# Performance work log

Measured on AMD Instinct MI355X. Metric: run time of the kernel, lower is better.

The kernel has to match this reference:

```python
import jax, jax.numpy as jnp
import numpy as np

V, E, H = 32000, 512, 1024
B, TS, TP = 32, 50, 32


def build_sparse_u_input(slot_np):
    # faithful jnp version of get_sparse_selective_input (vocab.decode EOS check skipped)
    ts, b = slot_np.shape
    res = jnp.full((ts, b, V + ts), 1e-10, dtype=jnp.float32)
    copy_mask = (slot_np == 2) | (slot_np >= V)
    add_mask = (slot_np != 0) & (~copy_mask)
    ti = jnp.arange(ts)[:, None]
    bi = jnp.arange(b)[None, :]
    res = res.at[ti, bi, slot_np].add(add_mask.astype(jnp.float32))
    res = res.at[ti, bi, V + ti].add((5.0 - 1e-10) * copy_mask.astype(jnp.float32))
    return jnp.transpose(res, (1, 0, 2))  # [B, Ts, V+Ts]


def setup_inputs() -> dict:
    key = jax.random.key(0)
    ks = jax.random.split(key, 20)
    s = lambda d: 1.0 / np.sqrt(d)
    slot_np = jax.random.randint(ks[0], (TS, B), 0, V)
    inp = {
        'slot_enc_out': jax.random.normal(ks[1], (TS, B, H), jnp.float32),
        'personality_enc_out': jax.random.normal(ks[2], (TP, B, H), jnp.float32),
        'last_hidden': jax.random.normal(ks[3], (1, B, H), jnp.float32),
        'm_t_input': jax.random.randint(ks[4], (1, B), 0, V),
        'slot_np': slot_np,
        'sparse_u_input': build_sparse_u_input(slot_np),
        'emb': jax.random.normal(ks[5], (V, E), jnp.float32),
        'W_attn_a': jax.random.normal(ks[6], (H, 2 * H), jnp.float32) * s(2 * H),
        'b_attn_a': jnp.zeros((H,), jnp.float32),
        'v_a': jax.random.normal(ks[7], (H,), jnp.float32) * s(H),
        'W_attn_p': jax.random.normal(ks[8], (H, 2 * H), jnp.float32) * s(2 * H),
        'b_attn_p': jnp.zeros((H,), jnp.float32),
        'v_p': jax.random.normal(ks[9], (H,), jnp.float32) * s(H),
        'W_ih': jax.random.normal(ks[10], (3 * H, E + 2 * H), jnp.float32) * s(E + 2 * H),
        'W_hh': jax.random.normal(ks[11], (3 * H, H), jnp.float32) * s(H),
        'b_ih': jnp.zeros((3 * H,), jnp.float32),
        'b_hh': jnp.zeros((3 * H,), jnp.float32),
        'W_proj': jax.random.normal(ks[12], (V, 3 * H), jnp.float32) * s(3 * H),
        'b_proj': jnp.zeros((V,), jnp.float32),
        'W_c2': jax.random.normal(ks[13], (H, H), jnp.float32) * s(H),
        'b_c2': jnp.zeros((H,), jnp.float32),
    }
    return inp


def _attn(hidden, enc, W, b, v):
    # hidden: [1,B,H], enc: [T,B,H] -> context [B,H]
    enc_b = jnp.swapaxes(enc, 0, 1)                       # [B,T,H]
    Hh = jnp.broadcast_to(hidden[0][:, None, :], enc_b.shape)
    e = jnp.tanh(jnp.concatenate([Hh, enc_b], -1) @ W.T + b)  # [B,T,H]
    a = jax.nn.softmax(jnp.einsum('bth,h->bt', e, v), axis=-1)
    return jnp.einsum('bt,bth->bh', a, enc_b)


def _gru_cell(x, h, W_ih, W_hh, b_ih, b_hh):
    gi = x @ W_ih.T + b_ih
    gh = h @ W_hh.T + b_hh
    ir, iz, inn = jnp.split(gi, 3, axis=-1)
    hr, hz, hn = jnp.split(gh, 3, axis=-1)
    r = jax.nn.sigmoid(ir + hr)
    z = jax.nn.sigmoid(iz + hz)
    n = jnp.tanh(inn + r * hn)
    return (1.0 - z) * n + z * h


def reference(slot_enc_out, personality_enc_out, last_hidden, m_t_input, slot_np,
              sparse_u_input, emb, W_attn_a, b_attn_a, v_a, W_attn_p, b_attn_p, v_p,
              W_ih, W_hh, b_ih, b_hh, W_proj, b_proj, W_c2, b_c2):
    m_embed = emb[m_t_input[0]]                                    # [B,E]
    a_ctx = _attn(last_hidden, slot_enc_out, W_attn_a, b_attn_a, v_a)
    p_ctx = _attn(last_hidden, personality_enc_out, W_attn_p, b_attn_p, v_p)
    gru_in = jnp.concatenate([m_embed, a_ctx, p_ctx], axis=-1)     # [B,E+2H]
    h_new = _gru_cell(gru_in, last_hidden[0], W_ih, W_hh, b_ih, b_hh)  # [B,H]
    gen_score = jnp.concatenate([a_ctx, p_ctx, h_new], -1) @ W_proj.T + b_proj  # [B,V]
    # copy score
    uc = jnp.tanh(jnp.swapaxes(slot_enc_out, 0, 1) @ W_c2.T + b_c2)  # [B,Ts,H]
    u = jnp.einsum('bth,bh->bt', uc, h_new)                          # [B,Ts]
    m = jnp.max(u, axis=1, keepdims=True)
    u = jnp.exp(u - m)
    u = jnp.log(jnp.einsum('bt,btv->bv', u, sparse_u_input)) + m     # [B,V+Ts]
    scores = jax.nn.softmax(jnp.concatenate([gen_score, u], axis=1), axis=1)
    gen, cp = scores[:, :V], scores[:, V:]
    proba = jnp.concatenate([gen + cp[:, :V], cp[:, V:]], axis=1)    # [B,V+Ts]
    return proba, h_new[None], h_new[None]
```

## Files before the change

### kernel.cpp

```cpp
#include <hip/hip_runtime.h>
#include <math.h>

static constexpr int V_   = 32000;
static constexpr int E_   = 512;
static constexpr int H_   = 1024;
static constexpr int B_   = 32;
static constexpr int TS_  = 50;
static constexpr int TP_  = 32;
static constexpr int VTS  = V_ + TS_;
static constexpr int H3   = 3 * H_;
static constexpr int GIN_ = E_ + 2 * H_;
static constexpr int NS   = 8;
static constexpr int SLE  = (VTS + NS - 1) / NS;
static constexpr int GSL  = V_ / NS;
static constexpr int PSK  = 12;

__global__ void zero_gather(float* __restrict__ extra,
                            const float* __restrict__ emb,
                            const int* __restrict__ mt,
                            float* __restrict__ gx)
{
    const int i = blockIdx.x * 256 + threadIdx.x;
    if (i < B_ * VTS) extra[i] = 0.f;
    if (i < B_ * E_) gx[i] = emb[(size_t)mt[i >> 9] * E_ + (i & 511)];
}

__device__ __forceinline__ void m32v2_tile(
    const float* __restrict__ A, int lda,
    const float* __restrict__ W, int ldw, int wko,
    int klen, int n0, float* __restrict__ po, int N)
{
    __shared__ float As[32][36];
    __shared__ float Ws[32][257];

    const int tid  = threadIdx.x;
    const int lane = tid & 63;
    const int wv   = tid >> 6;
    const int wq   = lane & 7;
    const int wg   = lane >> 3;
    const int am   = tid >> 3;
    const int aq   = tid & 7;

    float acc[8][4];
#pragma unroll
    for (int i = 0; i < 8; ++i)
#pragma unroll
        for (int j = 0; j < 4; ++j) acc[i][j] = 0.f;

    float4 a4 = *reinterpret_cast<const float4*>(A + (size_t)am * lda + 4 * aq);
    float4 w4[8];
#pragma unroll
    for (int i = 0; i < 8; ++i)
        w4[i] = *reinterpret_cast<const float4*>(
            W + (size_t)(n0 + wv * 64 + i * 8 + wg) * ldw + wko + 4 * wq);

    for (int kb = 0; kb < klen; kb += 32) {
        __syncthreads();
        As[4 * aq + 0][am] = a4.x; As[4 * aq + 1][am] = a4.y;
        As[4 * aq + 2][am] = a4.z; As[4 * aq + 3][am] = a4.w;
#pragma unroll
        for (int i = 0; i < 8; ++i) {
            const int col = wv * 64 + i * 8 + wg;
            Ws[4 * wq + 0][col] = w4[i].x; Ws[4 * wq + 1][col] = w4[i].y;
            Ws[4 * wq + 2][col] = w4[i].z; Ws[4 * wq + 3][col] = w4[i].w;
        }
        __syncthreads();
        if (kb + 32 < klen) {
            a4 = *reinterpret_cast<const float4*>(A + (size_t)am * lda + kb + 32 + 4 * aq);
#pragma unroll
            for (int i = 0; i < 8; ++i)
                w4[i] = *reinterpret_cast<const float4*>(
                    W + (size_t)(n0 + wv * 64 + i * 8 + wg) * ldw + wko + kb + 32 + 4 * wq);
        }
#pragma unroll 8
        for (int k = 0; k < 32; ++k) {
            const float4 a0 = *reinterpret_cast<const float4*>(&As[k][wv * 8]);
            const float4 a1 = *reinterpret_cast<const float4*>(&As[k][wv * 8 + 4]);
            const float av[8] = {a0.x, a0.y, a0.z, a0.w, a1.x, a1.y, a1.z, a1.w};
            const float w0 = Ws[k][lane];
            const float w1 = Ws[k][lane + 64];
            const float w2 = Ws[k][lane + 128];
            const float w3 = Ws[k][lane + 192];
#pragma unroll
            for (int i = 0; i < 8; ++i) {
                acc[i][0] = fmaf(av[i], w0, acc[i][0]);
                acc[i][1] = fmaf(av[i], w1, acc[i][1]);
                acc[i][2] = fmaf(av[i], w2, acc[i][2]);
                acc[i][3] = fmaf(av[i], w3, acc[i][3]);
            }
        }
    }
#pragma unroll
    for (int i = 0; i < 8; ++i) {
        float* op = po + (size_t)(wv * 8 + i) * N + n0;
#pragma unroll
        for (int j = 0; j < 4; ++j)
            op[lane + 64 * j] = acc[i][j];
    }
}

__global__ __launch_bounds__(256)
void gemm_hid(const float* __restrict__ hid,
              const float* __restrict__ Wa, const float* __restrict__ Wp,
              float* __restrict__ parts)
{
    const int z = blockIdx.z, y = blockIdx.y, n0 = blockIdx.x * 256;
    const float* W = z ? Wp : Wa;
    m32v2_tile(hid + y * 256, H_, W, 2 * H_, y * 256, 256, n0,
               parts + (size_t)(z * 4 + y) * B_ * H_, H_);
}

__global__ __launch_bounds__(256)
void gemm_pcg(const float* __restrict__ ctxa, const float* __restrict__ ctxp,
              const float* __restrict__ hid, const float* __restrict__ gx,
              const float* __restrict__ W_proj,
              const float* __restrict__ W_ih, const float* __restrict__ W_hh,
              float* __restrict__ partsP, float* __restrict__ partsG)
{
    const int bid = blockIdx.x;
    if (bid < 1000) {
        const int y = bid / 125, n0 = (bid % 125) * 256;
        const int slice = y >> 2, kq = y & 3;
        const float* A = slice ? ctxp : ctxa;
        m32v2_tile(A + kq * 256, H_, W_proj, H3, slice * 1024 + kq * 256,
                   256, n0, partsP + (size_t)y * B_ * V_, V_);
    } else {
        const int idx = bid - 1000;
        const int y = idx / 12, n0 = (idx % 12) * 256;
        const float* A; int lda; const float* W; int ldw; int wko; int klo;
        if (y < 2)       { klo = y * 256;        A = gx;   lda = E_; W = W_ih; ldw = GIN_; wko = klo; }
        else if (y < 6)  { klo = (y - 2) * 256;  A = ctxa; lda = H_; W = W_ih; ldw = GIN_; wko = 512 + klo; }
        else if (y < 10) { klo = (y - 6) * 256;  A = ctxp; lda = H_; W = W_ih; ldw = GIN_; wko = 1536 + klo; }
        else             { klo = (y - 10) * 256; A = hid;  lda = H_; W = W_hh; ldw = H_;   wko = klo; }
        m32v2_tile(A + klo, lda, W, ldw, wko, 256, n0,
                   partsG + (size_t)y * B_ * H3, H3);
    }
}

__global__ __launch_bounds__(256)
void gemm_projh(const float* __restrict__ hnew, const float* __restrict__ W_proj,
                float* __restrict__ partsP)
{
    const int y = blockIdx.y, n0 = blockIdx.x * 256;
    m32v2_tile(hnew + y * 256, H_, W_proj, H3, 2048 + y * 256,
               256, n0, partsP + (size_t)(8 + y) * B_ * V_, V_);
}

__global__ void reduce_gru(const float* __restrict__ parts,
                           const float* __restrict__ b_ih, const float* __restrict__ b_hh,
                           const float* __restrict__ hid,
                           float* __restrict__ hnew,
                           float* __restrict__ o2, float* __restrict__ o3)
{
    const int i = blockIdx.x * 256 + threadIdx.x;
    if (i >= B_ * H_) return;
    const int b = i >> 10, j = i & 1023;
    float gi[3], gh[3];
#pragma unroll
    for (int c = 0; c < 3; ++c) {
        float s = b_ih[c * H_ + j];
        for (int y = 0; y < 10; ++y)
            s += parts[((size_t)y * B_ + b) * H3 + c * H_ + j];
        gi[c] = s;
        float t = b_hh[c * H_ + j];
        for (int y = 10; y < 14; ++y)
            t += parts[((size_t)y * B_ + b) * H3 + c * H_ + j];
        gh[c] = t;
    }
    const float r = 1.f / (1.f + expf(-(gi[0] + gh[0])));
    const float z = 1.f / (1.f + expf(-(gi[1] + gh[1])));
    const float n = tanhf(gi[2] + r * gh[2]);
    const float o = (1.f - z) * n + z * hid[i];
    hnew[i] = o; o2[i] = o; o3[i] = o;
}

__global__ __launch_bounds__(256)
void gemm_tall84(const float* __restrict__ slot_enc, const float* __restrict__ pers_enc,
                 const float* __restrict__ W_attn_a, const float* __restrict__ W_attn_p,
                 const float* __restrict__ W_c2,
                 const float* __restrict__ b_attn_a, const float* __restrict__ b_attn_p,
                 const float* __restrict__ b_c2,
                 const float* __restrict__ v_a, const float* __restrict__ v_p,
                 const float* __restrict__ parts,
                 float* __restrict__ SA, float* __restrict__ SP, float* __restrict__ UCt)
{
    __shared__ float As[32][68];
    __shared__ float Ws[32][132];
    const int z = blockIdx.z;
    const float* A; const float* W; float* C; int M, ldw;
    if (z == 0)      { A = slot_enc; W = W_attn_a + H_; C = SA;  M = TS_ * B_; ldw = 2 * H_; }
    else if (z == 1) { A = pers_enc; W = W_attn_p + H_; C = SP;  M = TP_ * B_; ldw = 2 * H_; }
    else             { A = slot_enc; W = W_c2;          C = UCt; M = TS_ * B_; ldw = H_; }
    const int m0 = blockIdx.x * 64;
    if (m0 >= M) return;
    const int n0 = blockIdx.y * 128;
    const int tid = threadIdx.x;
    const int tym = tid >> 5;
    const int txn = tid & 31;
    const int sr = tid & 63, sh = tid >> 6;
    const int wr = tid & 127, wh = tid >> 7;

    float acc[8][4];
#pragma unroll
    for (int i = 0; i < 8; ++i)
#pragma unroll
        for (int j = 0; j < 4; ++j) acc[i][j] = 0.f;

    float4 a4[2], w4[4];
#pragma unroll
    for (int q = 0; q < 2; ++q)
        a4[q] = *reinterpret_cast<const float4*>(A + (size_t)(m0 + sr) * H_ + 8 * sh + 4 * q);
#pragma unroll
    for (int q = 0; q < 4; ++q)
        w4[q] = *reinterpret_cast<const float4*>(W + (size_t)(n0 + wr) * ldw + 16 * wh + 4 * q);

    for (int kb = 0; kb < H_; kb += 32) {
        __syncthreads();
#pragma unroll
        for (int q = 0; q < 2; ++q) {
            As[8 * sh + 4 * q + 0][sr] = a4[q].x; As[8 * sh + 4 * q + 1][sr] = a4[q].y;
            As[8 * sh + 4 * q + 2][sr] = a4[q].z; As[8 * sh + 4 * q + 3][sr] = a4[q].w;
        }
#pragma unroll
        for (int q = 0; q < 4; ++q) {
            Ws[16 * wh + 4 * q + 0][wr] = w4[q].x; Ws[16 * wh + 4 * q + 1][wr] = w4[q].y;
            Ws[16 * wh + 4 * q + 2][wr] = w4[q].z; Ws[16 * wh + 4 * q + 3][wr] = w4[q].w;
        }
        __syncthreads();
        if (kb + 32 < H_) {
#pragma unroll
            for (int q = 0; q < 2; ++q)
                a4[q] = *reinterpret_cast<const float4*>(A + (size_t)(m0 + sr) * H_ + kb + 32 + 8 * sh + 4 * q);
#pragma unroll
            for (int q = 0; q < 4; ++q)
                w4[q] = *reinterpret_cast<const float4*>(W + (size_t)(n0 + wr) * ldw + kb + 32 + 16 * wh + 4 * q);
        }
#pragma unroll 8
        for (int k = 0; k < 32; ++k) {
            const float4 a0 = *reinterpret_cast<const float4*>(&As[k][8 * tym]);
            const float4 a1 = *reinterpret_cast<const float4*>(&As[k][8 * tym + 4]);
            const float av[8] = {a0.x, a0.y, a0.z, a0.w, a1.x, a1.y, a1.z, a1.w};
            const float w0 = Ws[k][txn];
            const float w1 = Ws[k][txn + 32];
            const float w2 = Ws[k][txn + 64];
            const float w3 = Ws[k][txn + 96];
#pragma unroll
            for (int i = 0; i < 8; ++i) {
                acc[i][0] = fmaf(av[i], w0, acc[i][0]);
                acc[i][1] = fmaf(av[i], w1, acc[i][1]);
                acc[i][2] = fmaf(av[i], w2, acc[i][2]);
                acc[i][3] = fmaf(av[i], w3, acc[i][3]);
            }
        }
    }

    if (z < 2) {
        const float* bvec = z ? b_attn_p : b_attn_a;
        const float* vvec = z ? v_p : v_a;
        const float* pp = parts + (size_t)(z * 4) * B_ * H_;
#pragma unroll
        for (int i = 0; i < 8; ++i) {
            const int row = m0 + 8 * tym + i;
            const int b = row & 31;
#pragma unroll
            for (int j = 0; j < 4; ++j) {
                const int col = n0 + txn + 32 * j;
                float ha = bvec[col];
#pragma unroll
                for (int ss = 0; ss < 4; ++ss)
                    ha += pp[((size_t)ss * B_ + b) * H_ + col];
                C[(size_t)row * H_ + col] = tanhf(acc[i][j] + ha) * vvec[col];
            }
        }
    } else {
#pragma unroll
        for (int i = 0; i < 8; ++i) {
            const int row = m0 + 8 * tym + i;
#pragma unroll
            for (int j = 0; j < 4; ++j) {
                const int col = n0 + txn + 32 * j;
                C[(size_t)row * H_ + col] = tanhf(acc[i][j] + b_c2[col]);
            }
        }
    }
}

template <int T>
__device__ __forceinline__ void attn_body(const float* __restrict__ S,
                                          const float* __restrict__ enc,
                                          float* __restrict__ ctx, int b)
{
    const int tid  = threadIdx.x;
    const int wave = tid >> 6;
    const int lane = tid & 63;
    __shared__ float sc[64];
    __shared__ float aw[64];

    for (int t = wave; t < T; t += 8) {
        const float* e = S + ((size_t)t * B_ + b) * H_;
        float p = 0.f;
#pragma unroll
        for (int j = 0; j < H_ / 64; ++j) p += e[lane + 64 * j];
#pragma unroll
        for (int off = 32; off > 0; off >>= 1) p += __shfl_down(p, off);
        if (lane == 0) sc[t] = p;
    }
    __syncthreads();
    if (tid < 64) {
        const float x = (tid < T) ? sc[tid] : -3.4e38f;
        float mx = x;
#pragma unroll
        for (int off = 32; off > 0; off >>= 1) mx = fmaxf(mx, __shfl_xor(mx, off));
        const float ex = (tid < T) ? expf(x - mx) : 0.f;
        float sm = ex;
#pragma unroll
        for (int off = 32; off > 0; off >>= 1) sm += __shfl_xor(sm, off);
        aw[tid] = ex / sm;
    }
    __syncthreads();
    for (int k = tid; k < H_; k += 512) {
        float c = 0.f;
#pragma unroll 10
        for (int t = 0; t < T; ++t)
            c += aw[t] * enc[((size_t)t * B_ + b) * H_ + k];
        ctx[(size_t)b * H_ + k] = c;
    }
}

__global__ __launch_bounds__(512)
void attn_fused3(const float* __restrict__ SA, const float* __restrict__ SP,
                 const float* __restrict__ slot_enc, const float* __restrict__ pers_enc,
                 float* __restrict__ ctxa, float* __restrict__ ctxp)
{
    const int b = blockIdx.x;
    if (blockIdx.y == 0) attn_body<TS_>(SA, slot_enc, ctxa, b);
    else                 attn_body<TP_>(SP, pers_enc, ctxp, b);
}

__global__ __launch_bounds__(512)
void u_prep_scatter2(const float* __restrict__ UCt, const float* __restrict__ hn,
                     const int* __restrict__ slot_np,
                     float* __restrict__ mS, float* __restrict__ extra)
{
    const int b    = blockIdx.x;
    const int tid  = threadIdx.x;
    const int wave = tid >> 6;
    const int lane = tid & 63;
    __shared__ float su[64];
    __shared__ float eu_s[64];

    const float* h = hn + (size_t)b * H_;
    for (int t = wave; t < TS_; t += 8) {
        const float* r = UCt + ((size_t)t * B_ + b) * H_;
        float p = 0.f;
#pragma unroll
        for (int j = 0; j < H_ / 64; ++j)
            p += r[lane + 64 * j] * h[lane + 64 * j];
#pragma unroll
        for (int off = 32; off > 0; off >>= 1) p += __shfl_down(p, off);
        if (lane == 0) su[t] = p;
    }
    __syncthreads();
    if (tid < 64) {
        const float x = (tid < TS_) ? su[tid] : -3.4e38f;
        float mx = x;
#pragma unroll
        for (int off = 32; off > 0; off >>= 1) mx = fmaxf(mx, __shfl_xor(mx, off));
        const float ex = (tid < TS_) ? expf(x - mx) : 0.f;
        float sm = ex;
#pragma unroll
        for (int off = 32; off > 0; off >>= 1) sm += __shfl_xor(sm, off);
        eu_s[tid] = ex;
        if (tid == 0) { mS[b * 2] = mx; mS[b * 2 + 1] = sm; }
    }
    __syncthreads();
    if (tid < TS_) {
        const int sv = slot_np[tid * B_ + b];
        const float e = eu_s[tid];
        const bool copy = (sv == 2) || (sv >= V_);
        const bool add  = (sv != 0) && !copy;
        if (add)  atomicAdd(&extra[(size_t)b * VTS + sv], e);
        if (copy) atomicAdd(&extra[(size_t)b * VTS + V_ + tid], 5.0f * e);
    }
}

__device__ __forceinline__ float blk_reduce(float v, float* red, int tid, bool ismax)
{
    red[tid] = v; __syncthreads();
    for (int s = 128; s > 0; s >>= 1) {
        if (tid < s) red[tid] = ismax ? fmaxf(red[tid], red[tid + s]) : (red[tid] + red[tid + s]);
        __syncthreads();
    }
    const float r = red[0]; __syncthreads();
    return r;
}

__global__ __launch_bounds__(256)
void ph_max2g(const float* __restrict__ parts, const float* __restrict__ b_proj,
              const float* __restrict__ extra,
              float* __restrict__ gen,
              float* __restrict__ pgm, float* __restrict__ pzs,
              float* __restrict__ pem, float* __restrict__ pes)
{
    const int b = blockIdx.x, s = blockIdx.y, tid = threadIdx.x;
    __shared__ float red[256];
    const int g0 = s * GSL;

    float gv[16];
    float gm = -3.4e38f;
#pragma unroll
    for (int u = 0; u < 16; ++u) {
        const int loc = tid + 256 * u;
        float val = -3.4e38f;
        if (loc < GSL) {
            const int idx = g0 + loc;
            float ssum = 0.f;
#pragma unroll
            for (int ss = 0; ss < PSK; ++ss)
                ssum += parts[((size_t)ss * B_ + b) * V_ + idx];
            val = ssum + b_proj[idx];
            gen[(size_t)b * V_ + idx] = val;
            gm = fmaxf(gm, val);
        }
        gv[u] = val;
    }
    gm = blk_reduce(gm, red, tid, true);
    float zs = 0.f;
#pragma unroll
    for (int u = 0; u < 16; ++u)
        zs += expf(gv[u] - gm);
    zs = blk_reduce(zs, red, tid, false);

    const float* ex = extra + (size_t)b * VTS;
    const int e0 = s * SLE;
    const int e1 = (e0 + SLE < VTS) ? e0 + SLE : VTS;
    float em = 0.f, es = 0.f;
    for (int i = e0 + tid; i < e1; i += 256) { const float v = ex[i]; em = fmaxf(em, v); es += v; }
    em = blk_reduce(em, red, tid, true);
    es = blk_reduce(es, red, tid, false);
    if (tid == 0) {
        pgm[b * NS + s] = gm; pzs[b * NS + s] = zs;
        pem[b * NS + s] = em; pes[b * NS + s] = es;
    }
}

__global__ __launch_bounds__(256)
void ph_write2(const float* __restrict__ gen, const float* __restrict__ extra,
               const float* __restrict__ pgm, const float* __restrict__ pzs,
               const float* __restrict__ pem, const float* __restrict__ pes,
               const float* __restrict__ mS, float* __restrict__ proba)
{
    const int b = blockIdx.x, s = blockIdx.y, tid = threadIdx.x;
    const float mb   = mS[b * 2];
    const float Sb   = mS[b * 2 + 1];
    const float base = 1e-10f * Sb;

    float gm = -3.4e38f, em = 0.f;
#pragma unroll
    for (int k = 0; k < NS; ++k) {
        gm = fmaxf(gm, pgm[b * NS + k]);
        em = fmaxf(em, pem[b * NS + k]);
    }
    const float M = fmaxf(gm, mb + logf(base + em));
    float s1 = 0.f, s2 = 0.f;
#pragma unroll
    for (int k = 0; k < NS; ++k) {
        s1 += pzs[b * NS + k] * expf(pgm[b * NS + k] - M);
        s2 += pes[b * NS + k];
    }
    const float cs  = expf(mb - M);
    const float inv = 1.f / (s1 + cs * (base * VTS + s2));

    const float* g  = gen + (size_t)b * V_;
    const float* ex = extra + (size_t)b * VTS;
    float* o = proba + (size_t)b * VTS;
    const int e0 = s * SLE;
    const int e1 = (e0 + SLE < VTS) ? e0 + SLE : VTS;
    for (int i = e0 + tid; i < e1; i += 256) {
        const float cp = cs * (base + ex[i]) * inv;
        o[i] = (i < V_) ? (expf(g[i] - M) * inv + cp) : cp;
    }
}

extern "C" void kernel_launch(void* const* d_in, const int* in_sizes, int n_in,
                              void* d_out, int out_size, void* d_ws, size_t ws_size,
                              hipStream_t stream)
{
    const float* slot_enc = (const float*)d_in[0];
    const float* pers_enc = (const float*)d_in[1];
    const float* hid      = (const float*)d_in[2];
    const int*   mt       = (const int*)d_in[3];
    const int*   slot_np  = (const int*)d_in[4];
    const float* emb      = (const float*)d_in[6];
    const float* W_attn_a = (const float*)d_in[7];
    const float* b_attn_a = (const float*)d_in[8];
    const float* v_a      = (const float*)d_in[9];
    const float* W_attn_p = (const float*)d_in[10];
    const float* b_attn_p = (const float*)d_in[11];
    const float* v_p      = (const float*)d_in[12];
    const float* W_ih     = (const float*)d_in[13];
    const float* W_hh     = (const float*)d_in[14];
    const float* b_ih     = (const float*)d_in[15];
    const float* b_hh     = (const float*)d_in[16];
    const float* W_proj   = (const float*)d_in[17];
    const float* b_proj   = (const float*)d_in[18];
    const float* W_c2     = (const float*)d_in[19];
    const float* b_c2     = (const float*)d_in[20];
    float* out = (float*)d_out;

    float* w = (float*)d_ws;
    size_t off = 0;
    auto alloc = [&](size_t n) { float* p = w + off; off += n; return p; };
    float* SA    = alloc((size_t)TS_ * B_ * H_);
    float* SP    = alloc((size_t)TP_ * B_ * H_);
    float* UCt   = alloc((size_t)TS_ * B_ * H_);
    float* ctxa  = alloc((size_t)B_ * H_);
    float* ctxp  = alloc((size_t)B_ * H_);
    float* gx    = alloc((size_t)B_ * E_);
    float* hnew  = alloc((size_t)B_ * H_);
    float* gen   = alloc((size_t)B_ * V_);
    float* mS    = alloc((size_t)2 * B_);
    float* extra = alloc((size_t)B_ * VTS);
    float* pgm   = alloc((size_t)B_ * NS);
    float* pzs   = alloc((size_t)B_ * NS);
    float* pem   = alloc((size_t)B_ * NS);
    float* pes   = alloc((size_t)B_ * NS);
    float* partsP = alloc((size_t)PSK * B_ * V_);
    float* partsG = alloc((size_t)14 * B_ * H3);
    float* partsH = partsG;
    float* partsHd = alloc((size_t)8 * B_ * H_);

    const int o2 = B_ * VTS;
    const int o3 = o2 + B_ * H_;
    (void)partsH;

    zero_gather<<<(B_ * VTS + 255) / 256, 256, 0, stream>>>(extra, emb, mt, gx);

    gemm_hid<<<dim3(4, 4, 2), 256, 0, stream>>>(hid, W_attn_a, W_attn_p, partsHd);

    gemm_tall84<<<dim3(25, 8, 3), 256, 0, stream>>>(
        slot_enc, pers_enc, W_attn_a, W_attn_p, W_c2,
        b_attn_a, b_attn_p, b_c2, v_a, v_p, partsHd, SA, SP, UCt);

    attn_fused3<<<dim3(B_, 2), 512, 0, stream>>>(SA, SP, slot_enc, pers_enc, ctxa, ctxp);

    gemm_pcg<<<1168, 256, 0, stream>>>(ctxa, ctxp, hid, gx, W_proj, W_ih, W_hh, partsP, partsG);

    reduce_gru<<<(B_ * H_ + 255) / 256, 256, 0, stream>>>(partsG, b_ih, b_hh, hid, hnew, out + o2, out + o3);

    gemm_projh<<<dim3(125, 4), 256, 0, stream>>>(hnew, W_proj, partsP);

    u_prep_scatter2<<<B_, 512, 0, stream>>>(UCt, hnew, slot_np, mS, extra);

    ph_max2g<<<dim3(B_, NS), 256, 0, stream>>>(partsP, b_proj, extra, gen, pgm, pzs, pem, pes);
    ph_write2<<<dim3(B_, NS), 256, 0, stream>>>(gen, extra, pgm, pzs, pem, pes, mS, out);
}
```

Before: 403.7 us.

## Fuse small kernels and vectorize GEMM tile shared-memory reads and stores

```diff
diff --git a/kernel.cpp b/kernel.cpp
--- a/kernel.cpp
+++ b/kernel.cpp
@@ -14,16 +14,7 @@
 static constexpr int SLE  = (VTS + NS - 1) / NS;
 static constexpr int GSL  = V_ / NS;
 static constexpr int PSK  = 12;
-
-__global__ void zero_gather(float* __restrict__ extra,
-                            const float* __restrict__ emb,
-                            const int* __restrict__ mt,
-                            float* __restrict__ gx)
-{
-    const int i = blockIdx.x * 256 + threadIdx.x;
-    if (i < B_ * VTS) extra[i] = 0.f;
-    if (i < B_ * E_) gx[i] = emb[(size_t)mt[i >> 9] * E_ + (i & 511)];
-}
+static constexpr int NZB  = (B_ * VTS + 255) / 256;
 
 __device__ __forceinline__ void m32v2_tile(
     const float* __restrict__ A, int lda,
@@ -31,7 +22,7 @@
     int klen, int n0, float* __restrict__ po, int N)
 {
     __shared__ float As[32][36];
-    __shared__ float Ws[32][257];
+    __shared__ float Ws[32][256];
 
     const int tid  = threadIdx.x;
     const int lane = tid & 63;
@@ -77,37 +68,40 @@
             const float4 a0 = *reinterpret_cast<const float4*>(&As[k][wv * 8]);
             const float4 a1 = *reinterpret_cast<const float4*>(&As[k][wv * 8 + 4]);
             const float av[8] = {a0.x, a0.y, a0.z, a0.w, a1.x, a1.y, a1.z, a1.w};
-            const float w0 = Ws[k][lane];
-            const float w1 = Ws[k][lane + 64];
-            const float w2 = Ws[k][lane + 128];
-            const float w3 = Ws[k][lane + 192];
-#pragma unroll
-            for (int i = 0; i < 8; ++i) {
-                acc[i][0] = fmaf(av[i], w0, acc[i][0]);
-                acc[i][1] = fmaf(av[i], w1, acc[i][1]);
-                acc[i][2] = fmaf(av[i], w2, acc[i][2]);
-                acc[i][3] = fmaf(av[i], w3, acc[i][3]);
-            }
+            const float4 wf = *reinterpret_cast<const float4*>(&Ws[k][4 * lane]);
+            const float wvv[4] = {wf.x, wf.y, wf.z, wf.w};
+#pragma unroll
+            for (int i = 0; i < 8; ++i)
+#pragma unroll
+                for (int j = 0; j < 4; ++j)
+                    acc[i][j] = fmaf(av[i], wvv[j], acc[i][j]);
         }
     }
 #pragma unroll
     for (int i = 0; i < 8; ++i) {
-        float* op = po + (size_t)(wv * 8 + i) * N + n0;
-#pragma unroll
-        for (int j = 0; j < 4; ++j)
-            op[lane + 64 * j] = acc[i][j];
+        float4 o; o.x = acc[i][0]; o.y = acc[i][1]; o.z = acc[i][2]; o.w = acc[i][3];
+        *reinterpret_cast<float4*>(po + (size_t)(wv * 8 + i) * N + n0 + 4 * lane) = o;
     }
 }
 
 __global__ __launch_bounds__(256)
-void gemm_hid(const float* __restrict__ hid,
-              const float* __restrict__ Wa, const float* __restrict__ Wp,
-              float* __restrict__ parts)
-{
-    const int z = blockIdx.z, y = blockIdx.y, n0 = blockIdx.x * 256;
-    const float* W = z ? Wp : Wa;
-    m32v2_tile(hid + y * 256, H_, W, 2 * H_, y * 256, 256, n0,
-               parts + (size_t)(z * 4 + y) * B_ * H_, H_);
+void zg_hid(float* __restrict__ extra, const float* __restrict__ emb,
+            const int* __restrict__ mt, float* __restrict__ gx,
+            const float* __restrict__ hid,
+            const float* __restrict__ Wa, const float* __restrict__ Wp,
+            float* __restrict__ partsHd)
+{
+    const int bid = blockIdx.x;
+    if (bid < NZB) {
+        const int i = bid * 256 + threadIdx.x;
+        if (i < B_ * VTS) extra[i] = 0.f;
+        if (i < B_ * E_) gx[i] = emb[(size_t)mt[i >> 9] * E_ + (i & 511)];
+        return;
+    }
+    const int idx = bid - NZB;
+    const int z = idx >> 4, y = (idx >> 2) & 3, bx = idx & 3;
+    m32v2_tile(hid + y * 256, H_, z ? Wp : Wa, 2 * H_, y * 256, 256, bx * 256,
+               partsHd + (size_t)(z * 4 + y) * B_ * H_, H_);
 }
 
 __global__ __launch_bounds__(256)
@@ -118,32 +112,26 @@
               float* __restrict__ partsP, float* __restrict__ partsG)
 {
     const int bid = blockIdx.x;
+    const float* A; int lda; const float* W; int ldw; int wko;
+    float* po; int N; int n0;
     if (bid < 1000) {
-        const int y = bid / 125, n0 = (bid % 125) * 256;
+        const int y = bid / 125; n0 = (bid % 125) * 256;
         const int slice = y >> 2, kq = y & 3;
-        const float* A = slice ? ctxp : ctxa;
-        m32v2_tile(A + kq * 256, H_, W_proj, H3, slice * 1024 + kq * 256,
-                   256, n0, partsP + (size_t)y * B_ * V_, V_);
+        A = (slice ? ctxp : ctxa) + kq * 256; lda = H_;
+        W = W_proj; ldw = H3; wko = slice * 1024 + kq * 256;
+        po = partsP + (size_t)y * B_ * V_; N = V_;
     } else {
         const int idx = bid - 1000;
-        const int y = idx / 12, n0 = (idx % 12) * 256;
-        const float* A; int lda; const float* W; int ldw; int wko; int klo;
+        const int y = idx / 12; n0 = (idx % 12) * 256;
+        int klo;
         if (y < 2)       { klo = y * 256;        A = gx;   lda = E_; W = W_ih; ldw = GIN_; wko = klo; }
         else if (y < 6)  { klo = (y - 2) * 256;  A = ctxa; lda = H_; W = W_ih; ldw = GIN_; wko = 512 + klo; }
         else if (y < 10) { klo = (y - 6) * 256;  A = ctxp; lda = H_; W = W_ih; ldw = GIN_; wko = 1536 + klo; }
         else             { klo = (y - 10) * 256; A = hid;  lda = H_; W = W_hh; ldw = H_;   wko = klo; }
-        m32v2_tile(A + klo, lda, W, ldw, wko, 256, n0,
-                   partsG + (size_t)y * B_ * H3, H3);
-    }
-}
-
-__global__ __launch_bounds__(256)
-void gemm_projh(const float* __restrict__ hnew, const float* __restrict__ W_proj,
-                float* __restrict__ partsP)
-{
-    const int y = blockIdx.y, n0 = blockIdx.x * 256;
-    m32v2_tile(hnew + y * 256, H_, W_proj, H3, 2048 + y * 256,
-               256, n0, partsP + (size_t)(8 + y) * B_ * V_, V_);
+        A += klo;
+        po = partsG + (size_t)y * B_ * H3; N = H3;
+    }
+    m32v2_tile(A, lda, W, ldw, wko, 256, n0, po, N);
 }
 
 __global__ void reduce_gru(const float* __restrict__ parts,
@@ -185,7 +173,7 @@
                  float* __restrict__ SA, float* __restrict__ SP, float* __restrict__ UCt)
 {
     __shared__ float As[32][68];
-    __shared__ float Ws[32][132];
+    __shared__ float Ws[32][128];
     const int z = blockIdx.z;
     const float* A; const float* W; float* C; int M, ldw;
     if (z == 0)      { A = slot_enc; W = W_attn_a + H_; C = SA;  M = TS_ * B_; ldw = 2 * H_; }
@@ -240,47 +228,51 @@
             const float4 a0 = *reinterpret_cast<const float4*>(&As[k][8 * tym]);
             const float4 a1 = *reinterpret_cast<const float4*>(&As[k][8 * tym + 4]);
             const float av[8] = {a0.x, a0.y, a0.z, a0.w, a1.x, a1.y, a1.z, a1.w};
-            const float w0 = Ws[k][txn];
-            const float w1 = Ws[k][txn + 32];
-            const float w2 = Ws[k][txn + 64];
-            const float w3 = Ws[k][txn + 96];
-#pragma unroll
-            for (int i = 0; i < 8; ++i) {
-                acc[i][0] = fmaf(av[i], w0, acc[i][0]);
-                acc[i][1] = fmaf(av[i], w1, acc[i][1]);
-                acc[i][2] = fmaf(av[i], w2, acc[i][2]);
-                acc[i][3] = fmaf(av[i], w3, acc[i][3]);
-            }
-        }
-    }
-
+            const float4 wf = *reinterpret_cast<const float4*>(&Ws[k][4 * txn]);
+            const float wvv[4] = {wf.x, wf.y, wf.z, wf.w};
+#pragma unroll
+            for (int i = 0; i < 8; ++i)
+#pragma unroll
+                for (int j = 0; j < 4; ++j)
+                    acc[i][j] = fmaf(av[i], wvv[j], acc[i][j]);
+        }
+    }
+
+    const int colb = n0 + 4 * txn;
     if (z < 2) {
         const float* bvec = z ? b_attn_p : b_attn_a;
         const float* vvec = z ? v_p : v_a;
         const float* pp = parts + (size_t)(z * 4) * B_ * H_;
+        const float4 b4 = *reinterpret_cast<const float4*>(bvec + colb);
+        const float4 v4 = *reinterpret_cast<const float4*>(vvec + colb);
 #pragma unroll
         for (int i = 0; i < 8; ++i) {
             const int row = m0 + 8 * tym + i;
             const int b = row & 31;
-#pragma unroll
-            for (int j = 0; j < 4; ++j) {
-                const int col = n0 + txn + 32 * j;
-                float ha = bvec[col];
-#pragma unroll
-                for (int ss = 0; ss < 4; ++ss)
-                    ha += pp[((size_t)ss * B_ + b) * H_ + col];
-                C[(size_t)row * H_ + col] = tanhf(acc[i][j] + ha) * vvec[col];
+            float4 ha = b4;
+#pragma unroll
+            for (int ss = 0; ss < 4; ++ss) {
+                const float4 p4 = *reinterpret_cast<const float4*>(&pp[((size_t)ss * B_ + b) * H_ + colb]);
+                ha.x += p4.x; ha.y += p4.y; ha.z += p4.z; ha.w += p4.w;
             }
+            float4 o;
+            o.x = tanhf(acc[i][0] + ha.x) * v4.x;
+            o.y = tanhf(acc[i][1] + ha.y) * v4.y;
+            o.z = tanhf(acc[i][2] + ha.z) * v4.z;
+            o.w = tanhf(acc[i][3] + ha.w) * v4.w;
+            *reinterpret_cast<float4*>(C + (size_t)row * H_ + colb) = o;
         }
     } else {
+        const float4 b4 = *reinterpret_cast<const float4*>(b_c2 + colb);
 #pragma unroll
         for (int i = 0; i < 8; ++i) {
             const int row = m0 + 8 * tym + i;
-#pragma unroll
-            for (int j = 0; j < 4; ++j) {
-                const int col = n0 + txn + 32 * j;
-                C[(size_t)row * H_ + col] = tanhf(acc[i][j] + b_c2[col]);
-            }
+            float4 o;
+            o.x = tanhf(acc[i][0] + b4.x);
+            o.y = tanhf(acc[i][1] + b4.y);
+            o.z = tanhf(acc[i][2] + b4.z);
+            o.w = tanhf(acc[i][3] + b4.w);
+            *reinterpret_cast<float4*>(C + (size_t)row * H_ + colb) = o;
         }
     }
 }
@@ -337,20 +329,27 @@
     else                 attn_body<TP_>(SP, pers_enc, ctxp, b);
 }
 
-__global__ __launch_bounds__(512)
-void u_prep_scatter2(const float* __restrict__ UCt, const float* __restrict__ hn,
-                     const int* __restrict__ slot_np,
-                     float* __restrict__ mS, float* __restrict__ extra)
-{
-    const int b    = blockIdx.x;
+__global__ __launch_bounds__(256)
+void projh_uprep(const float* __restrict__ hnew, const float* __restrict__ W_proj,
+                 float* __restrict__ partsP,
+                 const float* __restrict__ UCt, const int* __restrict__ slot_np,
+                 float* __restrict__ mS, float* __restrict__ extra)
+{
+    if (blockIdx.x < 500) {
+        const int y = blockIdx.x / 125, n0 = (blockIdx.x % 125) * 256;
+        m32v2_tile(hnew + y * 256, H_, W_proj, H3, 2048 + y * 256, 256, n0,
+                   partsP + (size_t)(8 + y) * B_ * V_, V_);
+        return;
+    }
+    const int b    = blockIdx.x - 500;
     const int tid  = threadIdx.x;
     const int wave = tid >> 6;
     const int lane = tid & 63;
     __shared__ float su[64];
     __shared__ float eu_s[64];
 
-    const float* h = hn + (size_t)b * H_;
-    for (int t = wave; t < TS_; t += 8) {
+    const float* h = hnew + (size_t)b * H_;
+    for (int t = wave; t < TS_; t += 4) {
         const float* r = UCt + ((size_t)t * B_ + b) * H_;
         float p = 0.f;
 #pragma unroll
@@ -525,18 +524,14 @@
     float* pzs   = alloc((size_t)B_ * NS);
     float* pem   = alloc((size_t)B_ * NS);
     float* pes   = alloc((size_t)B_ * NS);
-    float* partsP = alloc((size_t)PSK * B_ * V_);
-    float* partsG = alloc((size_t)14 * B_ * H3);
-    float* partsH = partsG;
+    float* partsP  = alloc((size_t)PSK * B_ * V_);
+    float* partsG  = alloc((size_t)14 * B_ * H3);
     float* partsHd = alloc((size_t)8 * B_ * H_);
 
     const int o2 = B_ * VTS;
     const int o3 = o2 + B_ * H_;
-    (void)partsH;
-
-    zero_gather<<<(B_ * VTS + 255) / 256, 256, 0, stream>>>(extra, emb, mt, gx);
-
-    gemm_hid<<<dim3(4, 4, 2), 256, 0, stream>>>(hid, W_attn_a, W_attn_p, partsHd);
+
+    zg_hid<<<NZB + 32, 256, 0, stream>>>(extra, emb, mt, gx, hid, W_attn_a, W_attn_p, partsHd);
 
     gemm_tall84<<<dim3(25, 8, 3), 256, 0, stream>>>(
         slot_enc, pers_enc, W_attn_a, W_attn_p, W_c2,
@@ -548,9 +543,7 @@
 
     reduce_gru<<<(B_ * H_ + 255) / 256, 256, 0, stream>>>(partsG, b_ih, b_hh, hid, hnew, out + o2, out + o3);
 
-    gemm_projh<<<dim3(125, 4), 256, 0, stream>>>(hnew, W_proj, partsP);
-
-    u_prep_scatter2<<<B_, 512, 0, stream>>>(UCt, hnew, slot_np, mS, extra);
+    projh_uprep<<<532, 256, 0, stream>>>(hnew, W_proj, partsP, UCt, slot_np, mS, extra);
 
     ph_max2g<<<dim3(B_, NS), 256, 0, stream>>>(partsP, b_proj, extra, gen, pgm, pzs, pem, pes);
     ph_write2<<<dim3(B_, NS), 256, 0, stream>>>(gen, extra, pgm, pzs, pem, pes, mS, out);
```

Result: no change. 403.2 us (-0.1%).
